# Kernel tuning notes

Measured on AMD Instinct MI355X. Metric: run time of the kernel, lower is better.

Reference implementation:

```python
import jax, jax.numpy as jnp
import numpy as np

N = 50000          # num nodes
E = 800000         # num edges (before self-loops)
F_IN = 128         # num_node_features
HEADS = 8          # num_heads (layer 1)
F_HEAD = 16        # features_per_head
N_CLASSES = 32     # num_classes (layer 2, heads=1)
NEG_SLOPE = 0.2    # PyG GATConv default LeakyReLU slope


def setup_inputs() -> dict:
    key = jax.random.key(0)
    ks = jax.random.split(key, 9)
    x = jax.random.normal(ks[0], (N, F_IN), jnp.float32)
    src = jax.random.randint(ks[1], (E,), 0, N, dtype=jnp.int32)
    dst = jax.random.randint(ks[2], (E,), 0, N, dtype=jnp.int32)
    # layer 1 params
    W1 = jax.random.normal(ks[3], (F_IN, HEADS * F_HEAD), jnp.float32) / np.sqrt(F_IN).astype(np.float32)
    a_src1 = jax.random.normal(ks[4], (HEADS, F_HEAD), jnp.float32) * 0.1
    a_dst1 = jax.random.normal(ks[5], (HEADS, F_HEAD), jnp.float32) * 0.1
    b1 = jnp.zeros((HEADS * F_HEAD,), jnp.float32)  # bias_init = zeros_
    # layer 2 params (heads=1)
    W2 = jax.random.normal(ks[6], (HEADS * F_HEAD, N_CLASSES), jnp.float32) / np.sqrt(HEADS * F_HEAD).astype(np.float32)
    a_src2 = jax.random.normal(ks[7], (1, N_CLASSES), jnp.float32) * 0.1
    a_dst2 = jax.random.normal(ks[8], (1, N_CLASSES), jnp.float32) * 0.1
    b2 = jnp.zeros((N_CLASSES,), jnp.float32)
    return {"x": x, "src": src, "dst": dst,
            "W1": W1, "a_src1": a_src1, "a_dst1": a_dst1, "b1": b1,
            "W2": W2, "a_src2": a_src2, "a_dst2": a_dst2, "b2": b2}


def gat_conv(x, src, dst, W, a_src, a_dst, b, heads, feat):
    """PyG-style GATConv (concat=True, add_self_loops=True)."""
    h = (x @ W).reshape(N, heads, feat)                 # [N,H,F]
    al_src = jnp.sum(h * a_src, axis=-1)                # [N,H]
    al_dst = jnp.sum(h * a_dst, axis=-1)                # [N,H]
    loop = jnp.arange(N, dtype=src.dtype)
    s = jnp.concatenate([src, loop])                    # [E+N]
    d = jnp.concatenate([dst, loop])                    # [E+N]
    e = jax.nn.leaky_relu(al_src[s] + al_dst[d], NEG_SLOPE)   # [E+N,H]
    # numerically stable softmax over edges grouped by dst node
    m = jax.ops.segment_max(e, d, num_segments=N)       # [N,H]
    ex = jnp.exp(e - m[d])
    denom = jax.ops.segment_sum(ex, d, num_segments=N)  # [N,H]
    alpha = ex / denom[d]                               # [E+N,H]
    out = jax.ops.segment_sum(alpha[:, :, None] * h[s], d, num_segments=N)  # [N,H,F]
    return out.reshape(N, heads * feat) + b


def reference(x, src, dst, W1, a_src1, a_dst1, b1, W2, a_src2, a_dst2, b2):
    h = gat_conv(x, src, dst, W1, a_src1, a_dst1, b1, HEADS, F_HEAD)
    h = jax.nn.elu(h)
    h = gat_conv(h, src, dst, W2, a_src2, a_dst2, b2, 1, N_CLASSES)
    return jax.nn.log_softmax(h, axis=1)
```

## Files before the change

kernel.cpp:

```cpp
#include <hip/hip_runtime.h>

#define N_NODES   50000
#define N_EDGES   800000
#define NEG_SLOPE 0.2f
#define NBKT      256
#define NPB       196
#define EPB       3125

__device__ __forceinline__ float leaky(float x) {
    return x > 0.f ? x : x * NEG_SLOPE;
}

__device__ __forceinline__ unsigned short f2bf(float f) {
    unsigned int u = __float_as_uint(f);
    unsigned int r = (u + 0x7FFFu + ((u >> 16) & 1u)) >> 16;
    return (unsigned short)r;
}

__device__ __forceinline__ float2 bf2f2(unsigned int p) {
    return make_float2(__uint_as_float(p << 16),
                       __uint_as_float(p & 0xFFFF0000u));
}

__device__ __forceinline__ void fma4(float4& acc, const float4 a,
                                     const float4 w0, const float4 w1,
                                     const float4 w2, const float4 w3) {
    acc.x = fmaf(a.x, w0.x, fmaf(a.y, w1.x, fmaf(a.z, w2.x, fmaf(a.w, w3.x, acc.x))));
    acc.y = fmaf(a.x, w0.y, fmaf(a.y, w1.y, fmaf(a.z, w2.y, fmaf(a.w, w3.y, acc.y))));
    acc.z = fmaf(a.x, w0.z, fmaf(a.y, w1.z, fmaf(a.z, w2.z, fmaf(a.w, w3.z, acc.z))));
    acc.w = fmaf(a.x, w0.w, fmaf(a.y, w1.w, fmaf(a.z, w2.w, fmaf(a.w, w3.w, acc.w))));
}

__device__ __forceinline__ float dot4(const float4 a, const float4 b) {
    return a.x * b.x + a.y * b.y + a.z * b.z + a.w * b.w;
}

__global__ __launch_bounds__(256) void k_hist(const int* __restrict__ dst,
                                              int* __restrict__ hist_g) {
    __shared__ int h[NBKT];
    const int tid = threadIdx.x, blk = blockIdx.x;
    h[tid] = 0;
    __syncthreads();
    const int e0 = blk * EPB;
    for (int j = e0 + tid; j < e0 + EPB; j += 256)
        atomicAdd(&h[dst[j] / NPB], 1);
    __syncthreads();
    hist_g[tid * NBKT + blk] = h[tid];
}

__global__ __launch_bounds__(256) void k_scanA(const int* __restrict__ hist_g,
                                               int* __restrict__ offs,
                                               int* __restrict__ totals) {
    __shared__ int sc[256];
    const int b = blockIdx.x, tid = threadIdx.x;
    int v = hist_g[b * 256 + tid];
    sc[tid] = v;
    __syncthreads();
    for (int off = 1; off < 256; off <<= 1) {
        int add = (tid >= off) ? sc[tid - off] : 0;
        __syncthreads();
        sc[tid] += add;
        __syncthreads();
    }
    offs[b * 256 + tid] = sc[tid] - v;
    if (tid == 255) totals[b] = sc[255];
}

__global__ __launch_bounds__(256) void k_binscatter(const int* __restrict__ src,
                                                    const int* __restrict__ dst,
                                                    const int* __restrict__ offs,
                                                    const int* __restrict__ totals,
                                                    unsigned int* __restrict__ binned) {
    __shared__ int cur[NBKT];
    __shared__ int sc[NBKT];
    const int tid = threadIdx.x, blk = blockIdx.x;
    const int tv = totals[tid];
    sc[tid] = tv;
    __syncthreads();
    for (int off = 1; off < 256; off <<= 1) {
        int add = (tid >= off) ? sc[tid - off] : 0;
        __syncthreads();
        sc[tid] += add;
        __syncthreads();
    }
    cur[tid] = (sc[tid] - tv) + offs[tid * NBKT + blk];
    __syncthreads();
    const int e0 = blk * EPB;
    for (int j = e0 + tid; j < e0 + EPB; j += 256) {
        int d   = dst[j];
        int bkt = d / NPB;
        int dl  = d - bkt * NPB;
        int pos = atomicAdd(&cur[bkt], 1);
        binned[pos] = (unsigned int)src[j] | ((unsigned int)dl << 18);
    }
}

__global__ __launch_bounds__(256) void k_csr_fine(const unsigned int* __restrict__ binned,
                                                  const int* __restrict__ totals,
                                                  int* __restrict__ row_ptr,
                                                  int* __restrict__ csr) {
    __shared__ int cnt[256];
    __shared__ int sc[256];
    __shared__ int cur[256];
    const int b = blockIdx.x, tid = threadIdx.x;
    sc[tid] = totals[tid];
    __syncthreads();
    for (int off = 1; off < 256; off <<= 1) {
        int add = (tid >= off) ? sc[tid - off] : 0;
        __syncthreads();
        sc[tid] += add;
        __syncthreads();
    }
    const int start = (b == 0) ? 0 : sc[b - 1];
    const int end   = sc[b];
    cnt[tid] = 0;
    __syncthreads();
    for (int j = start + tid; j < end; j += 256)
        atomicAdd(&cnt[(binned[j] >> 18) & 255], 1);
    __syncthreads();
    const int v = cnt[tid];
    sc[tid] = v;
    __syncthreads();
    for (int off = 1; off < 256; off <<= 1) {
        int add = (tid >= off) ? sc[tid - off] : 0;
        __syncthreads();
        sc[tid] += add;
        __syncthreads();
    }
    const int excl = sc[tid] - v;
    cur[tid] = excl;
    const int node = b * NPB + tid;
    if (tid < NPB && node < N_NODES) row_ptr[node] = start + excl;
    if (b == NBKT - 1 && tid == 0)   row_ptr[N_NODES] = N_EDGES;
    __syncthreads();
    for (int j = start + tid; j < end; j += 256) {
        unsigned int p = binned[j];
        int dl  = (p >> 18) & 255;
        int pos = start + atomicAdd(&cur[dl], 1);
        csr[pos] = (int)(p & 0x3FFFFu);
    }
}

__global__ __launch_bounds__(256) void k_gemm1(
    const float* __restrict__ x, const float* __restrict__ W1,
    const float* __restrict__ a_src, const float* __restrict__ a_dst,
    unsigned short* __restrict__ h1b, float* __restrict__ al_src,
    float* __restrict__ al_dst)
{
    __shared__ float4 xs4[64 * 32];
    __shared__ float4 ws4[128 * 16];
    const int tid  = threadIdx.x;
    const int half = blockIdx.x & 1;
    const int row0 = (int)(blockIdx.x >> 1) * 64;
    const int tc   = tid & 15;
    const int tr   = tid >> 4;
    const float4* x4  = (const float4*)x;
    const float4* W14 = (const float4*)W1;

    #pragma unroll
    for (int p = 0; p < 8; ++p) {
        int i = tid + p * 256;
        int k = i >> 4, c4 = i & 15;
        ws4[k * 16 + c4] = W14[k * 32 + half * 16 + c4];
    }
    #pragma unroll
    for (int p = 0; p < 8; ++p) {
        int i = tid + p * 256;
        int r = i >> 5, k4 = i & 31;
        int gr = row0 + r; if (gr > N_NODES - 1) gr = N_NODES - 1;
        xs4[r * 32 + (k4 ^ ((r >> 2) & 7))] = x4[gr * 32 + k4];
    }
    __syncthreads();

    float4 acc[4];
    #pragma unroll
    for (int i = 0; i < 4; ++i) acc[i] = make_float4(0.f, 0.f, 0.f, 0.f);
    const int sw = tr & 7;
    #pragma unroll 2
    for (int k4 = 0; k4 < 32; ++k4) {
        float4 w0 = ws4[(4 * k4 + 0) * 16 + tc];
        float4 w1 = ws4[(4 * k4 + 1) * 16 + tc];
        float4 w2 = ws4[(4 * k4 + 2) * 16 + tc];
        float4 w3 = ws4[(4 * k4 + 3) * 16 + tc];
        const int kk = k4 ^ sw;
        #pragma unroll
        for (int i = 0; i < 4; ++i) {
            float4 a = xs4[(4 * tr + i) * 32 + kk];
            fma4(acc[i], a, w0, w1, w2, w3);
        }
    }

    const int c0   = half * 64 + 4 * tc;
    const int head = c0 >> 4;
    const float4 as4 = ((const float4*)a_src)[half * 16 + tc];
    const float4 ad4 = ((const float4*)a_dst)[half * 16 + tc];
    #pragma unroll
    for (int i = 0; i < 4; ++i) {
        int r = row0 + 4 * tr + i;
        if (r < N_NODES) {
            ((ushort4*)h1b)[r * 32 + half * 16 + tc] =
                make_ushort4(f2bf(acc[i].x), f2bf(acc[i].y),
                             f2bf(acc[i].z), f2bf(acc[i].w));
            float s = dot4(acc[i], as4);
            float d = dot4(acc[i], ad4);
            s += __shfl_xor(s, 1); s += __shfl_xor(s, 2);
            d += __shfl_xor(d, 1); d += __shfl_xor(d, 2);
            if ((tc & 3) == 0) {
                al_src[r * 8 + head] = s;
                al_dst[r * 8 + head] = d;
            }
        }
    }
}

__global__ __launch_bounds__(256) void k_agg1(
    const unsigned short* __restrict__ h1b, const float* __restrict__ al_src,
    const float* __restrict__ al_dst, const int* __restrict__ row_ptr,
    const int* __restrict__ csr_src, const float* __restrict__ b1,
    float* __restrict__ h2)
{
    const int n = blockIdx.x * 4 + (threadIdx.x >> 6);
    const int l    = threadIdx.x & 63;
    const int slot = l >> 4;
    const int f2   = l & 15;
    const int head = f2 >> 1;
    const uint4* h1q = (const uint4*)h1b;

    const float alD = al_dst[n * 8 + head];
    float denom = 0.f;
    float acc[8];
    #pragma unroll
    for (int i = 0; i < 8; ++i) acc[i] = 0.f;

    if (slot == 0) {
        float w = __expf(leaky(al_src[n * 8 + head] + alD));
        uint4 q = h1q[n * 16 + f2];
        float2 v0 = bf2f2(q.x), v1 = bf2f2(q.y), v2 = bf2f2(q.z), v3 = bf2f2(q.w);
        denom = w;
        acc[0] = w * v0.x; acc[1] = w * v0.y; acc[2] = w * v1.x; acc[3] = w * v1.y;
        acc[4] = w * v2.x; acc[5] = w * v2.y; acc[6] = w * v3.x; acc[7] = w * v3.y;
    }

    const int beg = row_ptr[n], end = row_ptr[n + 1];
    int j = beg + slot;
    for (; j + 4 < end; j += 8) {
        int sa = csr_src[j];
        int sb = csr_src[j + 4];
        float ala = al_src[sa * 8 + head];
        float alb = al_src[sb * 8 + head];
        uint4 qa = h1q[sa * 16 + f2];
        uint4 qb = h1q[sb * 16 + f2];
        float wa = __expf(leaky(ala + alD));
        float wb = __expf(leaky(alb + alD));
        denom += wa + wb;
        float2 a0 = bf2f2(qa.x), a1 = bf2f2(qa.y), a2 = bf2f2(qa.z), a3 = bf2f2(qa.w);
        acc[0] = fmaf(wa, a0.x, acc[0]); acc[1] = fmaf(wa, a0.y, acc[1]);
        acc[2] = fmaf(wa, a1.x, acc[2]); acc[3] = fmaf(wa, a1.y, acc[3]);
        acc[4] = fmaf(wa, a2.x, acc[4]); acc[5] = fmaf(wa, a2.y, acc[5]);
        acc[6] = fmaf(wa, a3.x, acc[6]); acc[7] = fmaf(wa, a3.y, acc[7]);
        float2 b0 = bf2f2(qb.x), b1v = bf2f2(qb.y), b2v = bf2f2(qb.z), b3 = bf2f2(qb.w);
        acc[0] = fmaf(wb, b0.x, acc[0]); acc[1] = fmaf(wb, b0.y, acc[1]);
        acc[2] = fmaf(wb, b1v.x, acc[2]); acc[3] = fmaf(wb, b1v.y, acc[3]);
        acc[4] = fmaf(wb, b2v.x, acc[4]); acc[5] = fmaf(wb, b2v.y, acc[5]);
        acc[6] = fmaf(wb, b3.x, acc[6]); acc[7] = fmaf(wb, b3.y, acc[7]);
    }
    if (j < end) {
        int s = csr_src[j];
        float w = __expf(leaky(al_src[s * 8 + head] + alD));
        uint4 q = h1q[s * 16 + f2];
        denom += w;
        float2 v0 = bf2f2(q.x), v1 = bf2f2(q.y), v2 = bf2f2(q.z), v3 = bf2f2(q.w);
        acc[0] = fmaf(w, v0.x, acc[0]); acc[1] = fmaf(w, v0.y, acc[1]);
        acc[2] = fmaf(w, v1.x, acc[2]); acc[3] = fmaf(w, v1.y, acc[3]);
        acc[4] = fmaf(w, v2.x, acc[4]); acc[5] = fmaf(w, v2.y, acc[5]);
        acc[6] = fmaf(w, v3.x, acc[6]); acc[7] = fmaf(w, v3.y, acc[7]);
    }

    #pragma unroll
    for (int i = 0; i < 8; ++i) {
        acc[i] += __shfl_xor(acc[i], 16);
        acc[i] += __shfl_xor(acc[i], 32);
    }
    denom += __shfl_xor(denom, 16);
    denom += __shfl_xor(denom, 32);

    if (slot == 0) {
        const float4 bA = ((const float4*)b1)[f2 * 2];
        const float4 bB = ((const float4*)b1)[f2 * 2 + 1];
        float inv = 1.f / denom;
        float o[8];
        o[0] = acc[0] * inv + bA.x; o[1] = acc[1] * inv + bA.y;
        o[2] = acc[2] * inv + bA.z; o[3] = acc[3] * inv + bA.w;
        o[4] = acc[4] * inv + bB.x; o[5] = acc[5] * inv + bB.y;
        o[6] = acc[6] * inv + bB.z; o[7] = acc[7] * inv + bB.w;
        #pragma unroll
        for (int i = 0; i < 8; ++i) o[i] = o[i] > 0.f ? o[i] : expm1f(o[i]);
        ((float4*)h2)[n * 32 + f2 * 2]     = make_float4(o[0], o[1], o[2], o[3]);
        ((float4*)h2)[n * 32 + f2 * 2 + 1] = make_float4(o[4], o[5], o[6], o[7]);
    }
}

__global__ __launch_bounds__(128) void k_gemm2(
    const float* __restrict__ h2, const float* __restrict__ W2,
    const float* __restrict__ a_src, const float* __restrict__ a_dst,
    unsigned short* __restrict__ t2b, float* __restrict__ al_src,
    float* __restrict__ al_dst)
{
    __shared__ float4 xs4[64 * 32];
    __shared__ float4 ws4[128 * 8];
    const int tid  = threadIdx.x;
    const int row0 = (int)blockIdx.x * 64;
    const int tc   = tid & 7;
    const int tr   = tid >> 3;
    const float4* h24 = (const float4*)h2;
    const float4* W24 = (const float4*)W2;

    #pragma unroll
    for (int p = 0; p < 8; ++p) {
        int i = tid + p * 128;
        ws4[i] = W24[i];
    }
    #pragma unroll
    for (int p = 0; p < 16; ++p) {
        int i = tid + p * 128;
        int r = i >> 5, k4 = i & 31;
        int gr = row0 + r; if (gr > N_NODES - 1) gr = N_NODES - 1;
        xs4[r * 32 + (k4 ^ ((r >> 2) & 7))] = h24[gr * 32 + k4];
    }
    __syncthreads();

    float4 acc[4];
    #pragma unroll
    for (int i = 0; i < 4; ++i) acc[i] = make_float4(0.f, 0.f, 0.f, 0.f);
    const int sw = tr & 7;
    #pragma unroll 2
    for (int k4 = 0; k4 < 32; ++k4) {
        float4 w0 = ws4[(4 * k4 + 0) * 8 + tc];
        float4 w1 = ws4[(4 * k4 + 1) * 8 + tc];
        float4 w2 = ws4[(4 * k4 + 2) * 8 + tc];
        float4 w3 = ws4[(4 * k4 + 3) * 8 + tc];
        const int kk = k4 ^ sw;
        #pragma unroll
        for (int i = 0; i < 4; ++i) {
            float4 a = xs4[(4 * tr + i) * 32 + kk];
            fma4(acc[i], a, w0, w1, w2, w3);
        }
    }

    const float4 as4 = ((const float4*)a_src)[tc];
    const float4 ad4 = ((const float4*)a_dst)[tc];
    #pragma unroll
    for (int i = 0; i < 4; ++i) {
        int r = row0 + 4 * tr + i;
        if (r < N_NODES) {
            ((ushort4*)t2b)[r * 8 + tc] =
                make_ushort4(f2bf(acc[i].x), f2bf(acc[i].y),
                             f2bf(acc[i].z), f2bf(acc[i].w));
            float s = dot4(acc[i], as4);
            float d = dot4(acc[i], ad4);
            s += __shfl_xor(s, 1); s += __shfl_xor(s, 2); s += __shfl_xor(s, 4);
            d += __shfl_xor(d, 1); d += __shfl_xor(d, 2); d += __shfl_xor(d, 4);
            if (tc == 0) {
                al_src[r] = s;
                al_dst[r] = d;
            }
        }
    }
}

__global__ __launch_bounds__(256) void k_agg2(
    const unsigned short* __restrict__ t2b, const float* __restrict__ al_src,
    const float* __restrict__ al_dst, const int* __restrict__ row_ptr,
    const int* __restrict__ csr_src, const float* __restrict__ b2,
    float* __restrict__ out)
{
    const int n = blockIdx.x * 4 + (threadIdx.x >> 6);
    const int l = threadIdx.x & 63;
    const int slot = l >> 4;
    const int f2   = l & 15;
    const unsigned int* t2u = (const unsigned int*)t2b;

    const float alD = al_dst[n];
    float denom = 0.f;
    float2 acc = make_float2(0.f, 0.f);
    if (slot == 0) {
        float w = __expf(leaky(al_src[n] + alD));
        float2 v = bf2f2(t2u[n * 16 + f2]);
        denom = w;
        acc = make_float2(w * v.x, w * v.y);
    }
    const int beg = row_ptr[n], end = row_ptr[n + 1];
    int j = beg + slot;
    for (; j + 4 < end; j += 8) {
        int sa = csr_src[j];
        int sb = csr_src[j + 4];
        float ala = al_src[sa];
        float alb = al_src[sb];
        unsigned int pa = t2u[sa * 16 + f2];
        unsigned int pb = t2u[sb * 16 + f2];
        float wa = __expf(leaky(ala + alD));
        float wb = __expf(leaky(alb + alD));
        denom += wa + wb;
        float2 va = bf2f2(pa), vb = bf2f2(pb);
        acc.x = fmaf(wa, va.x, acc.x); acc.y = fmaf(wa, va.y, acc.y);
        acc.x = fmaf(wb, vb.x, acc.x); acc.y = fmaf(wb, vb.y, acc.y);
    }
    if (j < end) {
        int s = csr_src[j];
        float w = __expf(leaky(al_src[s] + alD));
        float2 v = bf2f2(t2u[s * 16 + f2]);
        denom += w;
        acc.x = fmaf(w, v.x, acc.x);
        acc.y = fmaf(w, v.y, acc.y);
    }
    acc.x += __shfl_xor(acc.x, 16); acc.y += __shfl_xor(acc.y, 16);
    denom += __shfl_xor(denom, 16);
    acc.x += __shfl_xor(acc.x, 32); acc.y += __shfl_xor(acc.y, 32);
    denom += __shfl_xor(denom, 32);

    const float2 bb = ((const float2*)b2)[f2];
    float ox = acc.x / denom + bb.x;
    float oy = acc.y / denom + bb.y;
    float m = fmaxf(ox, oy);
    for (int off = 8; off; off >>= 1) m = fmaxf(m, __shfl_xor(m, off));
    float ssum = __expf(ox - m) + __expf(oy - m);
    for (int off = 8; off; off >>= 1) ssum += __shfl_xor(ssum, off);
    float lg = __logf(ssum);
    if (l < 16)
        ((float2*)out)[n * 16 + f2] = make_float2(ox - m - lg, oy - m - lg);
}

extern "C" void kernel_launch(void* const* d_in, const int* in_sizes, int n_in,
                              void* d_out, int out_size, void* d_ws, size_t ws_size,
                              hipStream_t stream) {
    const float* x      = (const float*)d_in[0];
    const int*   src    = (const int*)d_in[1];
    const int*   dst    = (const int*)d_in[2];
    const float* W1     = (const float*)d_in[3];
    const float* a_src1 = (const float*)d_in[4];
    const float* a_dst1 = (const float*)d_in[5];
    const float* b1     = (const float*)d_in[6];
    const float* W2     = (const float*)d_in[7];
    const float* a_src2 = (const float*)d_in[8];
    const float* a_dst2 = (const float*)d_in[9];
    const float* b2     = (const float*)d_in[10];
    float* out = (float*)d_out;

    char* ws = (char*)d_ws;
    size_t off = 0;
    auto alloc = [&](size_t bytes) {
        void* p = ws + off;
        off += (bytes + 255) & ~(size_t)255;
        return p;
    };
    unsigned short* h1b = (unsigned short*)alloc((size_t)N_NODES * 128 * 2);
    float*          h2  = (float*)alloc((size_t)N_NODES * 128 * 4);
    unsigned short* t2b = (unsigned short*)alloc((size_t)N_NODES * 32 * 2);
    float* alS1    = (float*)alloc((size_t)N_NODES * 8 * 4);
    float* alD1    = (float*)alloc((size_t)N_NODES * 8 * 4);
    float* alS2    = (float*)alloc((size_t)N_NODES * 4);
    float* alD2    = (float*)alloc((size_t)N_NODES * 4);
    int*   rowp    = (int*)alloc((size_t)(N_NODES + 1) * 4);
    int*   csr     = (int*)alloc((size_t)N_EDGES * 4);
    unsigned int* binned = (unsigned int*)alloc((size_t)N_EDGES * 4);
    int*   hist_g  = (int*)alloc((size_t)NBKT * NBKT * 4);
    int*   offs    = (int*)alloc((size_t)NBKT * NBKT * 4);
    int*   totals  = (int*)alloc((size_t)NBKT * 4);
    (void)ws_size; (void)in_sizes; (void)n_in; (void)out_size;

    const int row_tiles = (N_NODES + 63) / 64;

    k_hist<<<NBKT, 256, 0, stream>>>(dst, hist_g);
    k_scanA<<<NBKT, 256, 0, stream>>>(hist_g, offs, totals);
    k_binscatter<<<NBKT, 256, 0, stream>>>(src, dst, offs, totals, binned);
    k_csr_fine<<<NBKT, 256, 0, stream>>>(binned, totals, rowp, csr);
    k_gemm1<<<row_tiles * 2, 256, 0, stream>>>(x, W1, a_src1, a_dst1, h1b, alS1, alD1);
    k_agg1<<<N_NODES / 4, 256, 0, stream>>>(h1b, alS1, alD1, rowp, csr, b1, h2);
    k_gemm2<<<row_tiles, 128, 0, stream>>>(h2, W2, a_src2, a_dst2, t2b, alS2, alD2);
    k_agg2<<<N_NODES / 4, 256, 0, stream>>>(t2b, alS2, alD2, rowp, csr, b2, out);
}
```

Before: 233.3 us.

## Merge binscatter into gemm1 launch, unroll agg1 gather, widen agg2 lanes

The edge bin-scatter and the first-layer GEMM now run as one launch, with the first NBKT blocks doing the scatter, so independent work overlaps and one launch is dropped. The GEMM blocks now use a single 64KB shared buffer, which may lower occupancy for the scatter blocks. The layer-1 aggregation gains a four-edge unrolled loop so more gathers are in flight at once. Layer-2 aggregation switches to 8 edge slots with 4 features per lane and one reciprocal, changing the reduction and log-softmax shuffle pattern.

```diff
diff --git a/kernel.cpp b/kernel.cpp
--- a/kernel.cpp
+++ b/kernel.cpp
@@ -66,92 +66,49 @@
     if (tid == 255) totals[b] = sc[255];
 }
 
-__global__ __launch_bounds__(256) void k_binscatter(const int* __restrict__ src,
-                                                    const int* __restrict__ dst,
-                                                    const int* __restrict__ offs,
-                                                    const int* __restrict__ totals,
-                                                    unsigned int* __restrict__ binned) {
-    __shared__ int cur[NBKT];
-    __shared__ int sc[NBKT];
-    const int tid = threadIdx.x, blk = blockIdx.x;
-    const int tv = totals[tid];
-    sc[tid] = tv;
-    __syncthreads();
-    for (int off = 1; off < 256; off <<= 1) {
-        int add = (tid >= off) ? sc[tid - off] : 0;
-        __syncthreads();
-        sc[tid] += add;
-        __syncthreads();
-    }
-    cur[tid] = (sc[tid] - tv) + offs[tid * NBKT + blk];
-    __syncthreads();
-    const int e0 = blk * EPB;
-    for (int j = e0 + tid; j < e0 + EPB; j += 256) {
-        int d   = dst[j];
-        int bkt = d / NPB;
-        int dl  = d - bkt * NPB;
-        int pos = atomicAdd(&cur[bkt], 1);
-        binned[pos] = (unsigned int)src[j] | ((unsigned int)dl << 18);
-    }
-}
-
-__global__ __launch_bounds__(256) void k_csr_fine(const unsigned int* __restrict__ binned,
-                                                  const int* __restrict__ totals,
-                                                  int* __restrict__ row_ptr,
-                                                  int* __restrict__ csr) {
-    __shared__ int cnt[256];
-    __shared__ int sc[256];
-    __shared__ int cur[256];
-    const int b = blockIdx.x, tid = threadIdx.x;
-    sc[tid] = totals[tid];
-    __syncthreads();
-    for (int off = 1; off < 256; off <<= 1) {
-        int add = (tid >= off) ? sc[tid - off] : 0;
-        __syncthreads();
-        sc[tid] += add;
-        __syncthreads();
-    }
-    const int start = (b == 0) ? 0 : sc[b - 1];
-    const int end   = sc[b];
-    cnt[tid] = 0;
-    __syncthreads();
-    for (int j = start + tid; j < end; j += 256)
-        atomicAdd(&cnt[(binned[j] >> 18) & 255], 1);
-    __syncthreads();
-    const int v = cnt[tid];
-    sc[tid] = v;
-    __syncthreads();
-    for (int off = 1; off < 256; off <<= 1) {
-        int add = (tid >= off) ? sc[tid - off] : 0;
-        __syncthreads();
-        sc[tid] += add;
-        __syncthreads();
-    }
-    const int excl = sc[tid] - v;
-    cur[tid] = excl;
-    const int node = b * NPB + tid;
-    if (tid < NPB && node < N_NODES) row_ptr[node] = start + excl;
-    if (b == NBKT - 1 && tid == 0)   row_ptr[N_NODES] = N_EDGES;
-    __syncthreads();
-    for (int j = start + tid; j < end; j += 256) {
-        unsigned int p = binned[j];
-        int dl  = (p >> 18) & 255;
-        int pos = start + atomicAdd(&cur[dl], 1);
-        csr[pos] = (int)(p & 0x3FFFFu);
-    }
-}
-
-__global__ __launch_bounds__(256) void k_gemm1(
+__global__ __launch_bounds__(256) void k_bin_gemm1(
+    const int* __restrict__ src, const int* __restrict__ dst,
+    const int* __restrict__ offs, const int* __restrict__ totals,
+    unsigned int* __restrict__ binned,
     const float* __restrict__ x, const float* __restrict__ W1,
     const float* __restrict__ a_src, const float* __restrict__ a_dst,
     unsigned short* __restrict__ h1b, float* __restrict__ al_src,
     float* __restrict__ al_dst)
 {
-    __shared__ float4 xs4[64 * 32];
-    __shared__ float4 ws4[128 * 16];
-    const int tid  = threadIdx.x;
-    const int half = blockIdx.x & 1;
-    const int row0 = (int)(blockIdx.x >> 1) * 64;
+    __shared__ __align__(16) unsigned char smem[65536];
+    const int tid = threadIdx.x;
+
+    if (blockIdx.x < NBKT) {
+        int* cur = (int*)smem;
+        int* sc  = (int*)(smem + 1024);
+        const int blk = blockIdx.x;
+        const int tv = totals[tid];
+        sc[tid] = tv;
+        __syncthreads();
+        for (int off = 1; off < 256; off <<= 1) {
+            int add = (tid >= off) ? sc[tid - off] : 0;
+            __syncthreads();
+            sc[tid] += add;
+            __syncthreads();
+        }
+        cur[tid] = (sc[tid] - tv) + offs[tid * NBKT + blk];
+        __syncthreads();
+        const int e0 = blk * EPB;
+        for (int j = e0 + tid; j < e0 + EPB; j += 256) {
+            int d   = dst[j];
+            int bkt = d / NPB;
+            int dl  = d - bkt * NPB;
+            int pos = atomicAdd(&cur[bkt], 1);
+            binned[pos] = (unsigned int)src[j] | ((unsigned int)dl << 18);
+        }
+        return;
+    }
+
+    float4* xs4 = (float4*)smem;
+    float4* ws4 = (float4*)(smem + 32768);
+    const int bid  = (int)blockIdx.x - NBKT;
+    const int half = bid & 1;
+    const int row0 = (bid >> 1) * 64;
     const int tc   = tid & 15;
     const int tr   = tid >> 4;
     const float4* x4  = (const float4*)x;
@@ -213,6 +170,52 @@
     }
 }
 
+__global__ __launch_bounds__(256) void k_csr_fine(const unsigned int* __restrict__ binned,
+                                                  const int* __restrict__ totals,
+                                                  int* __restrict__ row_ptr,
+                                                  int* __restrict__ csr) {
+    __shared__ int cnt[256];
+    __shared__ int sc[256];
+    __shared__ int cur[256];
+    const int b = blockIdx.x, tid = threadIdx.x;
+    sc[tid] = totals[tid];
+    __syncthreads();
+    for (int off = 1; off < 256; off <<= 1) {
+        int add = (tid >= off) ? sc[tid - off] : 0;
+        __syncthreads();
+        sc[tid] += add;
+        __syncthreads();
+    }
+    const int start = (b == 0) ? 0 : sc[b - 1];
+    const int end   = sc[b];
+    cnt[tid] = 0;
+    __syncthreads();
+    for (int j = start + tid; j < end; j += 256)
+        atomicAdd(&cnt[(binned[j] >> 18) & 255], 1);
+    __syncthreads();
+    const int v = cnt[tid];
+    sc[tid] = v;
+    __syncthreads();
+    for (int off = 1; off < 256; off <<= 1) {
+        int add = (tid >= off) ? sc[tid - off] : 0;
+        __syncthreads();
+        sc[tid] += add;
+        __syncthreads();
+    }
+    const int excl = sc[tid] - v;
+    cur[tid] = excl;
+    const int node = b * NPB + tid;
+    if (tid < NPB && node < N_NODES) row_ptr[node] = start + excl;
+    if (b == NBKT - 1 && tid == 0)   row_ptr[N_NODES] = N_EDGES;
+    __syncthreads();
+    for (int j = start + tid; j < end; j += 256) {
+        unsigned int p = binned[j];
+        int dl  = (p >> 18) & 255;
+        int pos = start + atomicAdd(&cur[dl], 1);
+        csr[pos] = (int)(p & 0x3FFFFu);
+    }
+}
+
 __global__ __launch_bounds__(256) void k_agg1(
     const unsigned short* __restrict__ h1b, const float* __restrict__ al_src,
     const float* __restrict__ al_dst, const int* __restrict__ row_ptr,
@@ -243,6 +246,42 @@
 
     const int beg = row_ptr[n], end = row_ptr[n + 1];
     int j = beg + slot;
+    for (; j + 12 < end; j += 16) {
+        int s0 = csr_src[j];
+        int s1 = csr_src[j + 4];
+        int s2 = csr_src[j + 8];
+        int s3 = csr_src[j + 12];
+        float al0 = al_src[s0 * 8 + head];
+        float al1 = al_src[s1 * 8 + head];
+        float al2 = al_src[s2 * 8 + head];
+        float al3 = al_src[s3 * 8 + head];
+        uint4 q0 = h1q[s0 * 16 + f2];
+        uint4 q1 = h1q[s1 * 16 + f2];
+        uint4 q2 = h1q[s2 * 16 + f2];
+        uint4 q3 = h1q[s3 * 16 + f2];
+        float w0 = __expf(leaky(al0 + alD));
+        float w1 = __expf(leaky(al1 + alD));
+        float w2 = __expf(leaky(al2 + alD));
+        float w3 = __expf(leaky(al3 + alD));
+        denom += (w0 + w1) + (w2 + w3);
+        float2 v;
+        v = bf2f2(q0.x); acc[0] = fmaf(w0, v.x, acc[0]); acc[1] = fmaf(w0, v.y, acc[1]);
+        v = bf2f2(q0.y); acc[2] = fmaf(w0, v.x, acc[2]); acc[3] = fmaf(w0, v.y, acc[3]);
+        v = bf2f2(q0.z); acc[4] = fmaf(w0, v.x, acc[4]); acc[5] = fmaf(w0, v.y, acc[5]);
+        v = bf2f2(q0.w); acc[6] = fmaf(w0, v.x, acc[6]); acc[7] = fmaf(w0, v.y, acc[7]);
+        v = bf2f2(q1.x); acc[0] = fmaf(w1, v.x, acc[0]); acc[1] = fmaf(w1, v.y, acc[1]);
+        v = bf2f2(q1.y); acc[2] = fmaf(w1, v.x, acc[2]); acc[3] = fmaf(w1, v.y, acc[3]);
+        v = bf2f2(q1.z); acc[4] = fmaf(w1, v.x, acc[4]); acc[5] = fmaf(w1, v.y, acc[5]);
+        v = bf2f2(q1.w); acc[6] = fmaf(w1, v.x, acc[6]); acc[7] = fmaf(w1, v.y, acc[7]);
+        v = bf2f2(q2.x); acc[0] = fmaf(w2, v.x, acc[0]); acc[1] = fmaf(w2, v.y, acc[1]);
+        v = bf2f2(q2.y); acc[2] = fmaf(w2, v.x, acc[2]); acc[3] = fmaf(w2, v.y, acc[3]);
+        v = bf2f2(q2.z); acc[4] = fmaf(w2, v.x, acc[4]); acc[5] = fmaf(w2, v.y, acc[5]);
+        v = bf2f2(q2.w); acc[6] = fmaf(w2, v.x, acc[6]); acc[7] = fmaf(w2, v.y, acc[7]);
+        v = bf2f2(q3.x); acc[0] = fmaf(w3, v.x, acc[0]); acc[1] = fmaf(w3, v.y, acc[1]);
+        v = bf2f2(q3.y); acc[2] = fmaf(w3, v.x, acc[2]); acc[3] = fmaf(w3, v.y, acc[3]);
+        v = bf2f2(q3.z); acc[4] = fmaf(w3, v.x, acc[4]); acc[5] = fmaf(w3, v.y, acc[5]);
+        v = bf2f2(q3.w); acc[6] = fmaf(w3, v.x, acc[6]); acc[7] = fmaf(w3, v.y, acc[7]);
+    }
     for (; j + 4 < end; j += 8) {
         int sa = csr_src[j];
         int sb = csr_src[j + 4];
@@ -253,27 +292,26 @@
         float wa = __expf(leaky(ala + alD));
         float wb = __expf(leaky(alb + alD));
         denom += wa + wb;
-        float2 a0 = bf2f2(qa.x), a1 = bf2f2(qa.y), a2 = bf2f2(qa.z), a3 = bf2f2(qa.w);
-        acc[0] = fmaf(wa, a0.x, acc[0]); acc[1] = fmaf(wa, a0.y, acc[1]);
-        acc[2] = fmaf(wa, a1.x, acc[2]); acc[3] = fmaf(wa, a1.y, acc[3]);
-        acc[4] = fmaf(wa, a2.x, acc[4]); acc[5] = fmaf(wa, a2.y, acc[5]);
-        acc[6] = fmaf(wa, a3.x, acc[6]); acc[7] = fmaf(wa, a3.y, acc[7]);
-        float2 b0 = bf2f2(qb.x), b1v = bf2f2(qb.y), b2v = bf2f2(qb.z), b3 = bf2f2(qb.w);
-        acc[0] = fmaf(wb, b0.x, acc[0]); acc[1] = fmaf(wb, b0.y, acc[1]);
-        acc[2] = fmaf(wb, b1v.x, acc[2]); acc[3] = fmaf(wb, b1v.y, acc[3]);
-        acc[4] = fmaf(wb, b2v.x, acc[4]); acc[5] = fmaf(wb, b2v.y, acc[5]);
-        acc[6] = fmaf(wb, b3.x, acc[6]); acc[7] = fmaf(wb, b3.y, acc[7]);
+        float2 v;
+        v = bf2f2(qa.x); acc[0] = fmaf(wa, v.x, acc[0]); acc[1] = fmaf(wa, v.y, acc[1]);
+        v = bf2f2(qa.y); acc[2] = fmaf(wa, v.x, acc[2]); acc[3] = fmaf(wa, v.y, acc[3]);
+        v = bf2f2(qa.z); acc[4] = fmaf(wa, v.x, acc[4]); acc[5] = fmaf(wa, v.y, acc[5]);
+        v = bf2f2(qa.w); acc[6] = fmaf(wa, v.x, acc[6]); acc[7] = fmaf(wa, v.y, acc[7]);
+        v = bf2f2(qb.x); acc[0] = fmaf(wb, v.x, acc[0]); acc[1] = fmaf(wb, v.y, acc[1]);
+        v = bf2f2(qb.y); acc[2] = fmaf(wb, v.x, acc[2]); acc[3] = fmaf(wb, v.y, acc[3]);
+        v = bf2f2(qb.z); acc[4] = fmaf(wb, v.x, acc[4]); acc[5] = fmaf(wb, v.y, acc[5]);
+        v = bf2f2(qb.w); acc[6] = fmaf(wb, v.x, acc[6]); acc[7] = fmaf(wb, v.y, acc[7]);
     }
     if (j < end) {
         int s = csr_src[j];
         float w = __expf(leaky(al_src[s * 8 + head] + alD));
         uint4 q = h1q[s * 16 + f2];
         denom += w;
-        float2 v0 = bf2f2(q.x), v1 = bf2f2(q.y), v2 = bf2f2(q.z), v3 = bf2f2(q.w);
-        acc[0] = fmaf(w, v0.x, acc[0]); acc[1] = fmaf(w, v0.y, acc[1]);
-        acc[2] = fmaf(w, v1.x, acc[2]); acc[3] = fmaf(w, v1.y, acc[3]);
-        acc[4] = fmaf(w, v2.x, acc[4]); acc[5] = fmaf(w, v2.y, acc[5]);
-        acc[6] = fmaf(w, v3.x, acc[6]); acc[7] = fmaf(w, v3.y, acc[7]);
+        float2 v;
+        v = bf2f2(q.x); acc[0] = fmaf(w, v.x, acc[0]); acc[1] = fmaf(w, v.y, acc[1]);
+        v = bf2f2(q.y); acc[2] = fmaf(w, v.x, acc[2]); acc[3] = fmaf(w, v.y, acc[3]);
+        v = bf2f2(q.z); acc[4] = fmaf(w, v.x, acc[4]); acc[5] = fmaf(w, v.y, acc[5]);
+        v = bf2f2(q.w); acc[6] = fmaf(w, v.x, acc[6]); acc[7] = fmaf(w, v.y, acc[7]);
     }
 
     #pragma unroll
@@ -376,58 +414,67 @@
 {
     const int n = blockIdx.x * 4 + (threadIdx.x >> 6);
     const int l = threadIdx.x & 63;
-    const int slot = l >> 4;
-    const int f2   = l & 15;
-    const unsigned int* t2u = (const unsigned int*)t2b;
+    const int slot = l >> 3;
+    const int f4   = l & 7;
+    const uint2* t2u = (const uint2*)t2b;
 
     const float alD = al_dst[n];
     float denom = 0.f;
-    float2 acc = make_float2(0.f, 0.f);
+    float4 acc = make_float4(0.f, 0.f, 0.f, 0.f);
     if (slot == 0) {
         float w = __expf(leaky(al_src[n] + alD));
-        float2 v = bf2f2(t2u[n * 16 + f2]);
+        uint2 q = t2u[n * 8 + f4];
+        float2 v0 = bf2f2(q.x), v1 = bf2f2(q.y);
         denom = w;
-        acc = make_float2(w * v.x, w * v.y);
+        acc = make_float4(w * v0.x, w * v0.y, w * v1.x, w * v1.y);
     }
     const int beg = row_ptr[n], end = row_ptr[n + 1];
     int j = beg + slot;
-    for (; j + 4 < end; j += 8) {
+    for (; j + 8 < end; j += 16) {
         int sa = csr_src[j];
-        int sb = csr_src[j + 4];
+        int sb = csr_src[j + 8];
         float ala = al_src[sa];
         float alb = al_src[sb];
-        unsigned int pa = t2u[sa * 16 + f2];
-        unsigned int pb = t2u[sb * 16 + f2];
+        uint2 qa = t2u[sa * 8 + f4];
+        uint2 qb = t2u[sb * 8 + f4];
         float wa = __expf(leaky(ala + alD));
         float wb = __expf(leaky(alb + alD));
         denom += wa + wb;
-        float2 va = bf2f2(pa), vb = bf2f2(pb);
-        acc.x = fmaf(wa, va.x, acc.x); acc.y = fmaf(wa, va.y, acc.y);
-        acc.x = fmaf(wb, vb.x, acc.x); acc.y = fmaf(wb, vb.y, acc.y);
+        float2 v;
+        v = bf2f2(qa.x); acc.x = fmaf(wa, v.x, acc.x); acc.y = fmaf(wa, v.y, acc.y);
+        v = bf2f2(qa.y); acc.z = fmaf(wa, v.x, acc.z); acc.w = fmaf(wa, v.y, acc.w);
+        v = bf2f2(qb.x); acc.x = fmaf(wb, v.x, acc.x); acc.y = fmaf(wb, v.y, acc.y);
+        v = bf2f2(qb.y); acc.z = fmaf(wb, v.x, acc.z); acc.w = fmaf(wb, v.y, acc.w);
     }
     if (j < end) {
         int s = csr_src[j];
         float w = __expf(leaky(al_src[s] + alD));
-        float2 v = bf2f2(t2u[s * 16 + f2]);
+        uint2 q = t2u[s * 8 + f4];
         denom += w;
-        acc.x = fmaf(w, v.x, acc.x);
-        acc.y = fmaf(w, v.y, acc.y);
-    }
-    acc.x += __shfl_xor(acc.x, 16); acc.y += __shfl_xor(acc.y, 16);
-    denom += __shfl_xor(denom, 16);
-    acc.x += __shfl_xor(acc.x, 32); acc.y += __shfl_xor(acc.y, 32);
-    denom += __shfl_xor(denom, 32);
-
-    const float2 bb = ((const float2*)b2)[f2];
-    float ox = acc.x / denom + bb.x;
-    float oy = acc.y / denom + bb.y;
-    float m = fmaxf(ox, oy);
-    for (int off = 8; off; off >>= 1) m = fmaxf(m, __shfl_xor(m, off));
-    float ssum = __expf(ox - m) + __expf(oy - m);
-    for (int off = 8; off; off >>= 1) ssum += __shfl_xor(ssum, off);
-    float lg = __logf(ssum);
-    if (l < 16)
-        ((float2*)out)[n * 16 + f2] = make_float2(ox - m - lg, oy - m - lg);
+        float2 v;
+        v = bf2f2(q.x); acc.x = fmaf(w, v.x, acc.x); acc.y = fmaf(w, v.y, acc.y);
+        v = bf2f2(q.y); acc.z = fmaf(w, v.x, acc.z); acc.w = fmaf(w, v.y, acc.w);
+    }
+    #pragma unroll
+    for (int off = 8; off <= 32; off <<= 1) {
+        acc.x += __shfl_xor(acc.x, off); acc.y += __shfl_xor(acc.y, off);
+        acc.z += __shfl_xor(acc.z, off); acc.w += __shfl_xor(acc.w, off);
+        denom += __shfl_xor(denom, off);
+    }
+
+    const float4 bb = ((const float4*)b2)[f4];
+    float inv = 1.f / denom;
+    float o0 = acc.x * inv + bb.x;
+    float o1 = acc.y * inv + bb.y;
+    float o2 = acc.z * inv + bb.z;
+    float o3 = acc.w * inv + bb.w;
+    float m = fmaxf(fmaxf(o0, o1), fmaxf(o2, o3));
+    for (int off = 1; off <= 4; off <<= 1) m = fmaxf(m, __shfl_xor(m, off));
+    float ssum = __expf(o0 - m) + __expf(o1 - m) + __expf(o2 - m) + __expf(o3 - m);
+    for (int off = 1; off <= 4; off <<= 1) ssum += __shfl_xor(ssum, off);
+    float lg = m + __logf(ssum);
+    if (slot == 0)
+        ((float4*)out)[n * 8 + f4] = make_float4(o0 - lg, o1 - lg, o2 - lg, o3 - lg);
 }
 
 extern "C" void kernel_launch(void* const* d_in, const int* in_sizes, int n_in,
@@ -472,9 +519,10 @@
 
     k_hist<<<NBKT, 256, 0, stream>>>(dst, hist_g);
     k_scanA<<<NBKT, 256, 0, stream>>>(hist_g, offs, totals);
-    k_binscatter<<<NBKT, 256, 0, stream>>>(src, dst, offs, totals, binned);
+    k_bin_gemm1<<<NBKT + row_tiles * 2, 256, 0, stream>>>(
+        src, dst, offs, totals, binned,
+        x, W1, a_src1, a_dst1, h1b, alS1, alD1);
     k_csr_fine<<<NBKT, 256, 0, stream>>>(binned, totals, rowp, csr);
-    k_gemm1<<<row_tiles * 2, 256, 0, stream>>>(x, W1, a_src1, a_dst1, h1b, alS1, alD1);
     k_agg1<<<N_NODES / 4, 256, 0, stream>>>(h1b, alS1, alD1, rowp, csr, b1, h2);
     k_gemm2<<<row_tiles, 128, 0, stream>>>(h2, W2, a_src2, a_dst2, t2b, alS2, alD2);
     k_agg2<<<N_NODES / 4, 256, 0, stream>>>(t2b, alS2, alD2, rowp, csr, b2, out);
```

Result: faster. 223.6 us (-4.1%).
